# Kernel tuning notes

Hardware: AMD Instinct MI355X
Metric: run time of the kernel (lower is better)

## Reference

```python
import jax, jax.numpy as jnp
import numpy as np

HIDDEN = 1024

def setup_inputs() -> dict:
    key = jax.random.key(0)
    k1, k2, k3 = jax.random.split(key, 3)
    H = HIDDEN
    # xavier_uniform for [H, 4H] kernels: bound = sqrt(6/(H+4H))
    bound = float(np.sqrt(6.0 / (H + 4 * H)))
    x = jax.random.normal(k1, (32, 512, H), dtype=jnp.float32)
    input_kernel = jax.random.uniform(k2, (H, 4 * H), dtype=jnp.float32, minval=-bound, maxval=bound)
    hidden_kernel = jax.random.uniform(k3, (H, 4 * H), dtype=jnp.float32, minval=-bound, maxval=bound)
    bias = jnp.zeros((4 * H,), dtype=jnp.float32)
    return {"x": x, "input_kernel": input_kernel, "hidden_kernel": hidden_kernel, "bias": bias}

def _lstm(x, input_kernel, hidden_kernel, bias):
    B, S, H = x.shape
    # Precompute input projection for all timesteps as one big GEMM: [B,S,4H]
    xg = jnp.einsum('bsh,hg->bsg', x, input_kernel) + bias
    h0 = jnp.zeros((B, H), dtype=x.dtype)
    c0 = jnp.zeros((B, H), dtype=x.dtype)

    def step(carry, xg_t):
        h, c = carry
        gates = xg_t + h @ hidden_kernel  # [B, 4H]
        i_g, f_g, g_g, o_g = jnp.split(gates, 4, axis=-1)
        c = jax.nn.sigmoid(f_g) * c + jax.nn.sigmoid(i_g) * jnp.tanh(g_g)
        h = jax.nn.sigmoid(o_g) * jnp.tanh(c)
        return (h, c), h

    # scan over time axis: move S to leading dim
    (_, _), hs = jax.lax.scan(step, (h0, c0), jnp.swapaxes(xg, 0, 1))
    return jnp.swapaxes(hs, 0, 1)  # [B, S, H]

def reference(x, input_kernel, hidden_kernel, bias):
    return _lstm(x, input_kernel, hidden_kernel, bias)
```

## Files before the change

kernel.cpp:

```cpp
#include <hip/hip_runtime.h>


typedef __attribute__((ext_vector_type(4))) float f32x4_t;
typedef __attribute__((ext_vector_type(8))) short bf16x8_t;
typedef unsigned long long ull_t;

#define HID   1024
#define SLEN  512
#define NGATE 4096

#define XG_OFF    0ULL
#define RING_OFF  134217728ULL
#define WIT_OFF   167772160ULL
#define WHT_OFF   176160768ULL
#define FLAGS_OFF 184680448ULL
#define XB_OFF    RING_OFF

#define NBLK_B      256
#define FLAG_STRIDE 4
#define SLOT_SHORTS 32768

__device__ __forceinline__ unsigned short f2bf(float f) {
  unsigned u = __float_as_uint(f);
  u += 0x7fffu + ((u >> 16) & 1u);
  return (unsigned short)(u >> 16);
}
__device__ __forceinline__ float bf2f(unsigned short u) {
  return __uint_as_float(((unsigned)u) << 16);
}
__device__ __forceinline__ float fast_rcp(float x) { return __builtin_amdgcn_rcpf(x); }
__device__ __forceinline__ float sigmoid_f(float x) { return fast_rcp(1.f + __expf(-x)); }
__device__ __forceinline__ float tanh_f(float x) { return 1.f - 2.f * fast_rcp(1.f + __expf(2.f * x)); }

__global__ __launch_bounds__(256) void conv_x_bf16(const float* __restrict__ in,
                                                   unsigned short* __restrict__ out) {
  size_t i = (size_t)blockIdx.x * 256 + threadIdx.x;
  const float4* p = (const float4*)in;
  float4 v = p[i];
  ushort4 o;
  o.x = f2bf(v.x); o.y = f2bf(v.y); o.z = f2bf(v.z); o.w = f2bf(v.w);
  ((ushort4*)out)[i] = o;
}

__global__ void transpose_w_bf16(const float* __restrict__ in,
                                 unsigned short* __restrict__ out) {
  __shared__ float tile[32][33];
  int tx = threadIdx.x, ty = threadIdx.y;
  int n0 = blockIdx.x * 32, k0 = blockIdx.y * 32;
  #pragma unroll
  for (int i = 0; i < 4; i++)
    tile[ty + 8 * i][tx] = in[(size_t)(k0 + ty + 8 * i) * NGATE + n0 + tx];
  __syncthreads();
  #pragma unroll
  for (int i = 0; i < 4; i++)
    out[(size_t)(n0 + ty + 8 * i) * HID + k0 + tx] = f2bf(tile[tx][ty + 8 * i]);
}

__global__ void init_ws(unsigned* __restrict__ flags) {
  int i = (int)blockIdx.x * 256 + threadIdx.x;
  if (i < NBLK_B * FLAG_STRIDE) flags[i] = 0u;
}

__global__ __launch_bounds__(256) void gemm_xg(const unsigned short* __restrict__ A,
                                               const unsigned short* __restrict__ BT,
                                               unsigned short* __restrict__ C) {
  extern __shared__ char smem[];
  char* As = smem;
  char* Bs = smem + 10240;
  const int tid = threadIdx.x;
  const int lane = tid & 63, w = tid >> 6, q = lane >> 4, l16 = lane & 15;
  const int wm = w & 1, wn = w >> 1;
  const size_t m0 = (size_t)blockIdx.y * 128, n0 = (size_t)blockIdx.x * 128;

  f32x4_t acc[4][4];
  #pragma unroll
  for (int i = 0; i < 4; i++)
    #pragma unroll
    for (int j = 0; j < 4; j++) acc[i][j] = (f32x4_t){0.f, 0.f, 0.f, 0.f};

  for (int kk = 0; kk < 32; kk++) {
    const int k0 = kk * 32;
    #pragma unroll
    for (int h = 0; h < 2; h++) {
      int idx = tid + h * 256;
      int r = idx >> 2, ch = idx & 3;
      uint4 va = *(const uint4*)((const char*)A + ((m0 + r) * HID + k0) * 2 + ch * 16);
      *(uint4*)(As + r * 80 + ch * 16) = va;
      uint4 vb = *(const uint4*)((const char*)BT + ((n0 + r) * HID + k0) * 2 + ch * 16);
      *(uint4*)(Bs + r * 80 + ch * 16) = vb;
    }
    __syncthreads();
    bf16x8_t af[4], bf[4];
    #pragma unroll
    for (int mt = 0; mt < 4; mt++)
      af[mt] = *(const bf16x8_t*)(As + (wm * 64 + mt * 16 + l16) * 80 + q * 16);
    #pragma unroll
    for (int nt = 0; nt < 4; nt++)
      bf[nt] = *(const bf16x8_t*)(Bs + (wn * 64 + nt * 16 + l16) * 80 + q * 16);
    #pragma unroll
    for (int mt = 0; mt < 4; mt++)
      #pragma unroll
      for (int nt = 0; nt < 4; nt++)
        acc[mt][nt] = __builtin_amdgcn_mfma_f32_16x16x32_bf16(af[mt], bf[nt], acc[mt][nt], 0, 0, 0);
    __syncthreads();
  }

  unsigned short* cst = (unsigned short*)smem;
  #pragma unroll
  for (int mt = 0; mt < 4; mt++)
    #pragma unroll
    for (int nt = 0; nt < 4; nt++)
      #pragma unroll
      for (int r = 0; r < 4; r++) {
        int m = wm * 64 + mt * 16 + q * 4 + r;
        int n = wn * 64 + nt * 16 + l16;
        cst[m * 136 + n] = f2bf(acc[mt][nt][r]);
      }
  __syncthreads();
  #pragma unroll
  for (int i = 0; i < 8; i++) {
    int idx = tid + i * 256;
    int row = idx >> 4, ch = idx & 15;
    uint4 v = *(const uint4*)((const char*)cst + row * 272 + ch * 16);
    *(uint4*)((char*)C + ((m0 + row) * NGATE + n0) * 2 + ch * 16) = v;
  }
}

__global__ __launch_bounds__(256, 1) void lstm_persistent(
    const unsigned short* __restrict__ xg,
    const unsigned short* __restrict__ whT,
    const float* __restrict__ bias,
    float* __restrict__ out,
    unsigned short* ring,
    unsigned* flags) {
  __shared__ __align__(16) char h_lds[8 * 2064];
  __shared__ float gates[16 * 65];

  const int tid = threadIdx.x;
  const int lane = tid & 63, wv = tid >> 6, q = lane >> 4, l16 = lane & 15;
  const int g = blockIdx.x >> 6;
  const int m = blockIdx.x & 63;
  const int b_l = tid >> 4, j_l = tid & 15;

  bf16x8_t bfr[32];
  {
    const char* wrow = (const char*)whT +
        ((size_t)(wv * 1024 + m * 16 + l16) * HID) * 2 + q * 16;
    #pragma unroll
    for (int kk = 0; kk < 32; kk++)
      bfr[kk] = *(const bf16x8_t*)(wrow + kk * 64);
    #pragma unroll
    for (int kk = 0; kk < 32; kk++)
      asm volatile("" : "+v"(bfr[kk]));
  }
  float bsr[4];
  #pragma unroll
  for (int G = 0; G < 4; G++) bsr[G] = bias[G * 1024 + m * 16 + j_l];
  float c_st = 0.f;
  const char* arow = h_lds + (l16 & 7) * 2064 + q * 16;
  unsigned short* ring_g = ring + (size_t)g * 8192;
  unsigned* fl_g = flags + g * 64 * FLAG_STRIDE;

  for (int t = 0; t < SLEN; t++) {
    unsigned short xgv[4];
    if (tid < 128) {
      const unsigned short* p =
          xg + ((size_t)(g * 8 + b_l) * 512 + t) * 4096 + m * 16 + j_l;
      xgv[0] = p[0]; xgv[1] = p[1024]; xgv[2] = p[2048]; xgv[3] = p[3072];
    }
    if (t > 0) {
      if (tid < 64) {
        const unsigned* fp = fl_g + tid * FLAG_STRIDE;
        while (__hip_atomic_load(fp, __ATOMIC_RELAXED, __HIP_MEMORY_SCOPE_AGENT) < (unsigned)t)
          __builtin_amdgcn_s_sleep(1);
      }
      __syncthreads();
      asm volatile("" ::: "memory");
      {
        const char* src = (const char*)(ring_g + (size_t)(t - 1) * SLOT_SHORTS);
        uint4 v0 = *(const uint4*)(src + tid * 16);
        uint4 v1 = *(const uint4*)(src + tid * 16 + 4096);
        uint4 v2 = *(const uint4*)(src + tid * 16 + 8192);
        uint4 v3 = *(const uint4*)(src + tid * 16 + 12288);
        int c0 = tid, c1 = tid + 256, c2 = tid + 512, c3 = tid + 768;
        *(uint4*)(h_lds + (c0 >> 7) * 2064 + (c0 & 127) * 16) = v0;
        *(uint4*)(h_lds + (c1 >> 7) * 2064 + (c1 & 127) * 16) = v1;
        *(uint4*)(h_lds + (c2 >> 7) * 2064 + (c2 & 127) * 16) = v2;
        *(uint4*)(h_lds + (c3 >> 7) * 2064 + (c3 & 127) * 16) = v3;
      }
    }
    __syncthreads();

    f32x4_t acc0 = (f32x4_t){0.f, 0.f, 0.f, 0.f};
    f32x4_t acc1 = (f32x4_t){0.f, 0.f, 0.f, 0.f};
    if (t > 0) {
      #pragma unroll
      for (int kk = 0; kk < 32; kk += 2) {
        bf16x8_t a0 = *(const bf16x8_t*)(arow + kk * 64);
        bf16x8_t a1 = *(const bf16x8_t*)(arow + kk * 64 + 64);
        acc0 = __builtin_amdgcn_mfma_f32_16x16x32_bf16(a0, bfr[kk], acc0, 0, 0, 0);
        acc1 = __builtin_amdgcn_mfma_f32_16x16x32_bf16(a1, bfr[kk + 1], acc1, 0, 0, 0);
      }
    }
    #pragma unroll
    for (int r = 0; r < 4; r++) {
      int bb = q * 4 + r;
      gates[bb * 65 + wv * 16 + l16] = acc0[r] + acc1[r];
    }
    __syncthreads();

    if (tid < 128) {
      float gi = gates[b_l * 65 + j_l]      + bsr[0] + bf2f(xgv[0]);
      float gf = gates[b_l * 65 + 16 + j_l] + bsr[1] + bf2f(xgv[1]);
      float gg = gates[b_l * 65 + 32 + j_l] + bsr[2] + bf2f(xgv[2]);
      float go = gates[b_l * 65 + 48 + j_l] + bsr[3] + bf2f(xgv[3]);
      float i_s = sigmoid_f(gi), f_s = sigmoid_f(gf);
      float g_t = tanh_f(gg), o_s = sigmoid_f(go);
      c_st = f_s * c_st + i_s * g_t;
      float h = o_s * tanh_f(c_st);
      unsigned short hb = f2bf(h);
      unsigned other = __shfl_xor((unsigned)hb, 1);
      unsigned u = ((unsigned)hb & 0xffffu) | (other << 16);
      unsigned u2 = __shfl_xor(u, 2);
      if ((j_l & 3) == 0) {
        ull_t v8 = (ull_t)u | ((ull_t)u2 << 32);
        ull_t* dst = (ull_t*)(ring_g + (size_t)t * SLOT_SHORTS +
                              b_l * 1024 + m * 16 + j_l);
        __hip_atomic_store(dst, v8, __ATOMIC_RELAXED, __HIP_MEMORY_SCOPE_AGENT);
      }
      asm volatile("" ::: "memory");
      out[((size_t)(g * 8 + b_l) * 512 + t) * 1024 + m * 16 + j_l] = h;
    }
    asm volatile("s_waitcnt vmcnt(1)" ::: "memory");
    __syncthreads();
    if (tid == 0)
      __hip_atomic_store(fl_g + m * FLAG_STRIDE, (unsigned)(t + 1),
                         __ATOMIC_RELAXED, __HIP_MEMORY_SCOPE_AGENT);
  }
}

extern "C" void kernel_launch(void* const* d_in, const int* in_sizes, int n_in,
                              void* d_out, int out_size, void* d_ws, size_t ws_size,
                              hipStream_t stream) {
  const float* x    = (const float*)d_in[0];
  const float* wi   = (const float*)d_in[1];
  const float* wh   = (const float*)d_in[2];
  const float* bias = (const float*)d_in[3];
  float* out = (float*)d_out;

  char* ws = (char*)d_ws;
  unsigned short* xg   = (unsigned short*)(ws + XG_OFF);
  unsigned short* xb   = (unsigned short*)(ws + XB_OFF);
  unsigned short* ring = (unsigned short*)(ws + RING_OFF);
  unsigned short* wiT  = (unsigned short*)(ws + WIT_OFF);
  unsigned short* whT  = (unsigned short*)(ws + WHT_OFF);
  unsigned* flags      = (unsigned*)(ws + FLAGS_OFF);

  conv_x_bf16<<<16384, 256, 0, stream>>>(x, xb);
  transpose_w_bf16<<<dim3(128, 32), dim3(32, 8), 0, stream>>>(wi, wiT);
  transpose_w_bf16<<<dim3(128, 32), dim3(32, 8), 0, stream>>>(wh, whT);
  init_ws<<<4, 256, 0, stream>>>(flags);
  gemm_xg<<<dim3(32, 128), 256, 34816, stream>>>(xb, wiT, xg);
  lstm_persistent<<<NBLK_B, 256, 0, stream>>>(xg, whT, bias, out, ring, flags);
}
```

Before: 1.930 ms.

## Split recurrent matmul over K across waves and pack flags densely

Each wave now owns one quarter of the K dimension for all four gates, instead of one gate over the full K. It writes partial sums to LDS, and the gate threads then reduce those four partials. This gives each wave four independent MFMA accumulation chains of length 8 rather than two chains of length 16, which shortens the serial MFMA dependency on the per-timestep critical path. It also packs the sync flags contiguously instead of padding them to a stride of 4, which trades possible false sharing for fewer cache lines polled per step.

```diff
diff --git a/kernel.cpp b/kernel.cpp
--- a/kernel.cpp
+++ b/kernel.cpp
@@ -17,7 +17,6 @@
 #define XB_OFF    RING_OFF
 
 #define NBLK_B      256
-#define FLAG_STRIDE 4
 #define SLOT_SHORTS 32768
 
 __device__ __forceinline__ unsigned short f2bf(float f) {
@@ -57,8 +56,8 @@
 }
 
 __global__ void init_ws(unsigned* __restrict__ flags) {
-  int i = (int)blockIdx.x * 256 + threadIdx.x;
-  if (i < NBLK_B * FLAG_STRIDE) flags[i] = 0u;
+  int i = threadIdx.x;
+  flags[i] = 0u;
 }
 
 __global__ __launch_bounds__(256) void gemm_xg(const unsigned short* __restrict__ A,
@@ -134,7 +133,7 @@
     unsigned short* ring,
     unsigned* flags) {
   __shared__ __align__(16) char h_lds[8 * 2064];
-  __shared__ float gates[16 * 65];
+  __shared__ float gatesp[4][8][68];
 
   const int tid = threadIdx.x;
   const int lane = tid & 63, wv = tid >> 6, q = lane >> 4, l16 = lane & 15;
@@ -144,11 +143,14 @@
 
   bf16x8_t bfr[32];
   {
-    const char* wrow = (const char*)whT +
-        ((size_t)(wv * 1024 + m * 16 + l16) * HID) * 2 + q * 16;
-    #pragma unroll
-    for (int kk = 0; kk < 32; kk++)
-      bfr[kk] = *(const bf16x8_t*)(wrow + kk * 64);
+    #pragma unroll
+    for (int G = 0; G < 4; G++) {
+      const char* wrow = (const char*)whT +
+          ((size_t)(G * 1024 + m * 16 + l16) * HID) * 2 + q * 16;
+      #pragma unroll
+      for (int i = 0; i < 8; i++)
+        bfr[G * 8 + i] = *(const bf16x8_t*)(wrow + (wv * 8 + i) * 64);
+    }
     #pragma unroll
     for (int kk = 0; kk < 32; kk++)
       asm volatile("" : "+v"(bfr[kk]));
@@ -159,7 +161,7 @@
   float c_st = 0.f;
   const char* arow = h_lds + (l16 & 7) * 2064 + q * 16;
   unsigned short* ring_g = ring + (size_t)g * 8192;
-  unsigned* fl_g = flags + g * 64 * FLAG_STRIDE;
+  unsigned* fl_g = flags + g * 64;
 
   for (int t = 0; t < SLEN; t++) {
     unsigned short xgv[4];
@@ -170,7 +172,7 @@
     }
     if (t > 0) {
       if (tid < 64) {
-        const unsigned* fp = fl_g + tid * FLAG_STRIDE;
+        const unsigned* fp = fl_g + tid;
         while (__hip_atomic_load(fp, __ATOMIC_RELAXED, __HIP_MEMORY_SCOPE_AGENT) < (unsigned)t)
           __builtin_amdgcn_s_sleep(1);
       }
@@ -191,29 +193,41 @@
     }
     __syncthreads();
 
-    f32x4_t acc0 = (f32x4_t){0.f, 0.f, 0.f, 0.f};
-    f32x4_t acc1 = (f32x4_t){0.f, 0.f, 0.f, 0.f};
+    f32x4_t acc[4];
+    #pragma unroll
+    for (int G = 0; G < 4; G++) acc[G] = (f32x4_t){0.f, 0.f, 0.f, 0.f};
     if (t > 0) {
       #pragma unroll
-      for (int kk = 0; kk < 32; kk += 2) {
-        bf16x8_t a0 = *(const bf16x8_t*)(arow + kk * 64);
-        bf16x8_t a1 = *(const bf16x8_t*)(arow + kk * 64 + 64);
-        acc0 = __builtin_amdgcn_mfma_f32_16x16x32_bf16(a0, bfr[kk], acc0, 0, 0, 0);
-        acc1 = __builtin_amdgcn_mfma_f32_16x16x32_bf16(a1, bfr[kk + 1], acc1, 0, 0, 0);
-      }
-    }
-    #pragma unroll
-    for (int r = 0; r < 4; r++) {
-      int bb = q * 4 + r;
-      gates[bb * 65 + wv * 16 + l16] = acc0[r] + acc1[r];
+      for (int i = 0; i < 8; i++) {
+        bf16x8_t a = *(const bf16x8_t*)(arow + (wv * 8 + i) * 64);
+        acc[0] = __builtin_amdgcn_mfma_f32_16x16x32_bf16(a, bfr[0 * 8 + i], acc[0], 0, 0, 0);
+        acc[1] = __builtin_amdgcn_mfma_f32_16x16x32_bf16(a, bfr[1 * 8 + i], acc[1], 0, 0, 0);
+        acc[2] = __builtin_amdgcn_mfma_f32_16x16x32_bf16(a, bfr[2 * 8 + i], acc[2], 0, 0, 0);
+        acc[3] = __builtin_amdgcn_mfma_f32_16x16x32_bf16(a, bfr[3 * 8 + i], acc[3], 0, 0, 0);
+      }
+    }
+    if (q < 2) {
+      #pragma unroll
+      for (int G = 0; G < 4; G++)
+        #pragma unroll
+        for (int r = 0; r < 4; r++)
+          gatesp[wv][q * 4 + r][G * 16 + l16] = acc[G][r];
     }
     __syncthreads();
 
     if (tid < 128) {
-      float gi = gates[b_l * 65 + j_l]      + bsr[0] + bf2f(xgv[0]);
-      float gf = gates[b_l * 65 + 16 + j_l] + bsr[1] + bf2f(xgv[1]);
-      float gg = gates[b_l * 65 + 32 + j_l] + bsr[2] + bf2f(xgv[2]);
-      float go = gates[b_l * 65 + 48 + j_l] + bsr[3] + bf2f(xgv[3]);
+      float gi = gatesp[0][b_l][j_l]      + gatesp[1][b_l][j_l]
+               + gatesp[2][b_l][j_l]      + gatesp[3][b_l][j_l]
+               + bsr[0] + bf2f(xgv[0]);
+      float gf = gatesp[0][b_l][16 + j_l] + gatesp[1][b_l][16 + j_l]
+               + gatesp[2][b_l][16 + j_l] + gatesp[3][b_l][16 + j_l]
+               + bsr[1] + bf2f(xgv[1]);
+      float gg = gatesp[0][b_l][32 + j_l] + gatesp[1][b_l][32 + j_l]
+               + gatesp[2][b_l][32 + j_l] + gatesp[3][b_l][32 + j_l]
+               + bsr[2] + bf2f(xgv[2]);
+      float go = gatesp[0][b_l][48 + j_l] + gatesp[1][b_l][48 + j_l]
+               + gatesp[2][b_l][48 + j_l] + gatesp[3][b_l][48 + j_l]
+               + bsr[3] + bf2f(xgv[3]);
       float i_s = sigmoid_f(gi), f_s = sigmoid_f(gf);
       float g_t = tanh_f(gg), o_s = sigmoid_f(go);
       c_st = f_s * c_st + i_s * g_t;
@@ -234,7 +248,7 @@
     asm volatile("s_waitcnt vmcnt(1)" ::: "memory");
     __syncthreads();
     if (tid == 0)
-      __hip_atomic_store(fl_g + m * FLAG_STRIDE, (unsigned)(t + 1),
+      __hip_atomic_store(fl_g + m, (unsigned)(t + 1),
                          __ATOMIC_RELAXED, __HIP_MEMORY_SCOPE_AGENT);
   }
 }
@@ -259,7 +273,7 @@
   conv_x_bf16<<<16384, 256, 0, stream>>>(x, xb);
   transpose_w_bf16<<<dim3(128, 32), dim3(32, 8), 0, stream>>>(wi, wiT);
   transpose_w_bf16<<<dim3(128, 32), dim3(32, 8), 0, stream>>>(wh, whT);
-  init_ws<<<4, 256, 0, stream>>>(flags);
+  init_ws<<<1, 256, 0, stream>>>(flags);
   gemm_xg<<<dim3(32, 128), 256, 34816, stream>>>(xb, wiT, xg);
   lstm_persistent<<<NBLK_B, 256, 0, stream>>>(xg, whT, bias, out, ring, flags);
 }
```

Measured after the change: 2.196 ms. 1.14x slower.

## Read recurrent h directly from global ring, drop LDS staging, pack flags

Applied to the files above, without the earlier changes.

The per-step staging of the previous hidden state from the global ring into LDS is removed. Each wave now loads its MFMA A-fragments straight from the ring buffer in four software-pipelined batches interleaved with the MFMAs, which also removes one block barrier per timestep. Flags are packed contiguously instead of padded with a stride of four. The risk is redundant global/L2 reads across waves, since every wave re-reads the same h, plus higher register pressure and false sharing on the packed flags.

```diff
diff --git a/kernel.cpp b/kernel.cpp
--- a/kernel.cpp
+++ b/kernel.cpp
@@ -17,7 +17,6 @@
 #define XB_OFF    RING_OFF
 
 #define NBLK_B      256
-#define FLAG_STRIDE 4
 #define SLOT_SHORTS 32768
 
 __device__ __forceinline__ unsigned short f2bf(float f) {
@@ -57,8 +56,8 @@
 }
 
 __global__ void init_ws(unsigned* __restrict__ flags) {
-  int i = (int)blockIdx.x * 256 + threadIdx.x;
-  if (i < NBLK_B * FLAG_STRIDE) flags[i] = 0u;
+  int i = threadIdx.x;
+  flags[i] = 0u;
 }
 
 __global__ __launch_bounds__(256) void gemm_xg(const unsigned short* __restrict__ A,
@@ -126,6 +125,20 @@
   }
 }
 
+#define LD8(dst, base_kk)                                                     \
+  _Pragma("unroll")                                                           \
+  for (int i_ = 0; i_ < 8; i_++)                                              \
+    dst[i_] = *(const bf16x8_t*)(ab + (base_kk) * 64 + i_ * 64);
+
+#define FM8(src, base_kk)                                                     \
+  _Pragma("unroll")                                                           \
+  for (int i_ = 0; i_ < 4; i_++) {                                            \
+    acc0 = __builtin_amdgcn_mfma_f32_16x16x32_bf16(src[2 * i_],               \
+             bfr[(base_kk) + 2 * i_], acc0, 0, 0, 0);                         \
+    acc1 = __builtin_amdgcn_mfma_f32_16x16x32_bf16(src[2 * i_ + 1],           \
+             bfr[(base_kk) + 2 * i_ + 1], acc1, 0, 0, 0);                     \
+  }
+
 __global__ __launch_bounds__(256, 1) void lstm_persistent(
     const unsigned short* __restrict__ xg,
     const unsigned short* __restrict__ whT,
@@ -133,7 +146,6 @@
     float* __restrict__ out,
     unsigned short* ring,
     unsigned* flags) {
-  __shared__ __align__(16) char h_lds[8 * 2064];
   __shared__ float gates[16 * 65];
 
   const int tid = threadIdx.x;
@@ -157,9 +169,9 @@
   #pragma unroll
   for (int G = 0; G < 4; G++) bsr[G] = bias[G * 1024 + m * 16 + j_l];
   float c_st = 0.f;
-  const char* arow = h_lds + (l16 & 7) * 2064 + q * 16;
   unsigned short* ring_g = ring + (size_t)g * 8192;
-  unsigned* fl_g = flags + g * 64 * FLAG_STRIDE;
+  unsigned* fl_g = flags + g * 64;
+  const int a_off = (l16 & 7) * 2048 + q * 16;
 
   for (int t = 0; t < SLEN; t++) {
     unsigned short xgv[4];
@@ -168,39 +180,22 @@
           xg + ((size_t)(g * 8 + b_l) * 512 + t) * 4096 + m * 16 + j_l;
       xgv[0] = p[0]; xgv[1] = p[1024]; xgv[2] = p[2048]; xgv[3] = p[3072];
     }
+    f32x4_t acc0 = (f32x4_t){0.f, 0.f, 0.f, 0.f};
+    f32x4_t acc1 = (f32x4_t){0.f, 0.f, 0.f, 0.f};
     if (t > 0) {
       if (tid < 64) {
-        const unsigned* fp = fl_g + tid * FLAG_STRIDE;
+        const unsigned* fp = fl_g + tid;
         while (__hip_atomic_load(fp, __ATOMIC_RELAXED, __HIP_MEMORY_SCOPE_AGENT) < (unsigned)t)
           __builtin_amdgcn_s_sleep(1);
       }
       __syncthreads();
       asm volatile("" ::: "memory");
-      {
-        const char* src = (const char*)(ring_g + (size_t)(t - 1) * SLOT_SHORTS);
-        uint4 v0 = *(const uint4*)(src + tid * 16);
-        uint4 v1 = *(const uint4*)(src + tid * 16 + 4096);
-        uint4 v2 = *(const uint4*)(src + tid * 16 + 8192);
-        uint4 v3 = *(const uint4*)(src + tid * 16 + 12288);
-        int c0 = tid, c1 = tid + 256, c2 = tid + 512, c3 = tid + 768;
-        *(uint4*)(h_lds + (c0 >> 7) * 2064 + (c0 & 127) * 16) = v0;
-        *(uint4*)(h_lds + (c1 >> 7) * 2064 + (c1 & 127) * 16) = v1;
-        *(uint4*)(h_lds + (c2 >> 7) * 2064 + (c2 & 127) * 16) = v2;
-        *(uint4*)(h_lds + (c3 >> 7) * 2064 + (c3 & 127) * 16) = v3;
-      }
-    }
-    __syncthreads();
-
-    f32x4_t acc0 = (f32x4_t){0.f, 0.f, 0.f, 0.f};
-    f32x4_t acc1 = (f32x4_t){0.f, 0.f, 0.f, 0.f};
-    if (t > 0) {
-      #pragma unroll
-      for (int kk = 0; kk < 32; kk += 2) {
-        bf16x8_t a0 = *(const bf16x8_t*)(arow + kk * 64);
-        bf16x8_t a1 = *(const bf16x8_t*)(arow + kk * 64 + 64);
-        acc0 = __builtin_amdgcn_mfma_f32_16x16x32_bf16(a0, bfr[kk], acc0, 0, 0, 0);
-        acc1 = __builtin_amdgcn_mfma_f32_16x16x32_bf16(a1, bfr[kk + 1], acc1, 0, 0, 0);
-      }
+      const char* ab = (const char*)(ring_g + (size_t)(t - 1) * SLOT_SHORTS) + a_off;
+      bf16x8_t af0[8], af1[8], af2[8], af3[8];
+      LD8(af0, 0);  LD8(af1, 8);
+      FM8(af0, 0);  LD8(af2, 16);
+      FM8(af1, 8);  LD8(af3, 24);
+      FM8(af2, 16); FM8(af3, 24);
     }
     #pragma unroll
     for (int r = 0; r < 4; r++) {
@@ -234,7 +229,7 @@
     asm volatile("s_waitcnt vmcnt(1)" ::: "memory");
     __syncthreads();
     if (tid == 0)
-      __hip_atomic_store(fl_g + m * FLAG_STRIDE, (unsigned)(t + 1),
+      __hip_atomic_store(fl_g + m, (unsigned)(t + 1),
                          __ATOMIC_RELAXED, __HIP_MEMORY_SCOPE_AGENT);
   }
 }
@@ -259,7 +254,7 @@
   conv_x_bf16<<<16384, 256, 0, stream>>>(x, xb);
   transpose_w_bf16<<<dim3(128, 32), dim3(32, 8), 0, stream>>>(wi, wiT);
   transpose_w_bf16<<<dim3(128, 32), dim3(32, 8), 0, stream>>>(wh, whT);
-  init_ws<<<4, 256, 0, stream>>>(flags);
+  init_ws<<<1, 256, 0, stream>>>(flags);
   gemm_xg<<<dim3(32, 128), 256, 34816, stream>>>(xb, wiT, xg);
   lstm_persistent<<<NBLK_B, 256, 0, stream>>>(xg, whT, bias, out, ring, flags);
 }
```

Result: slower. 4.546 ms (+135.5%).
